# Kernel optimization log

Hardware: AMD Instinct MI355X
Metric: run time of the kernel (lower is better)

The kernel has to match this reference:

```python
import jax, jax.numpy as jnp
import numpy as np

H = 512   # d_model (hidden)
L = 2     # rnn_layer_dim
E = 321   # enc_in
C = 321   # c_out (must equal enc_in: decoder output is fed back as input)
T = 96    # seq_len
P = 96    # pred_len
B = 512   # batch


def _cell(x, h, c, Wih, Whh, bih, bhh):
    # PyTorch LSTM gate order: input, forget, cell(g), output
    g = x @ Wih.T + h @ Whh.T + bih + bhh
    i, f, gg, o = jnp.split(g, 4, axis=-1)
    c = jax.nn.sigmoid(f) * c + jax.nn.sigmoid(i) * jnp.tanh(gg)
    h = jax.nn.sigmoid(o) * jnp.tanh(c)
    return h, c


def _run_layer(xs, Wih, Whh, bih, bhh):
    # xs: [T, B, in_dim] -> ys: [T, B, H], final (h, c)
    b = xs.shape[1]
    h0 = jnp.zeros((b, Whh.shape[1]), xs.dtype)
    def step(carry, x):
        h, c = carry
        h, c = _cell(x, h, c, Wih, Whh, bih, bhh)
        return (h, c), h
    (h, c), ys = jax.lax.scan(step, (h0, h0), xs)
    return ys, h, c


def _forward(x_enc, x_mark_enc, x_dec, x_mark_dec,
             e_Wih0, e_Whh0, e_bih0, e_bhh0, e_Wih1, e_Whh1, e_bih1, e_bhh1,
             d_Wih0, d_Whh0, d_bih0, d_bhh0, d_Wih1, d_Whh1, d_bih1, d_bhh1,
             fc_W, fc_b):
    del x_mark_enc, x_dec, x_mark_dec  # unused in use_tf=False path
    xs = jnp.swapaxes(x_enc, 0, 1)                     # [T, B, E]
    ys, h0, c0 = _run_layer(xs, e_Wih0, e_Whh0, e_bih0, e_bhh0)
    _,  h1, c1 = _run_layer(ys, e_Wih1, e_Whh1, e_bih1, e_bhh1)

    inp0 = x_enc[:, -1, :]                             # [B, E] last source step

    def dec_step(carry, _):
        inp, h0, c0, h1, c1 = carry
        h0, c0 = _cell(inp, h0, c0, d_Wih0, d_Whh0, d_bih0, d_bhh0)
        h1, c1 = _cell(h0,  h1, c1, d_Wih1, d_Whh1, d_bih1, d_bhh1)
        out = h1 @ fc_W.T + fc_b                       # [B, C]
        return (out, h0, c0, h1, c1), out

    _, outs = jax.lax.scan(dec_step, (inp0, h0, c0, h1, c1), None, length=P)
    return jnp.swapaxes(outs, 0, 1)                    # [B, P, C]


def setup_inputs() -> dict:
    key = jax.random.key(0)
    ks = jax.random.split(key, 24)
    s = 1.0 / np.sqrt(H)  # PyTorch LSTM init scale
    def w(k, shape):
        return jax.random.uniform(k, shape, jnp.float32, -s, s)
    inp = {
        "x_enc": jax.random.normal(ks[0], (B, T, E), jnp.float32),
        "x_mark_enc": jax.random.normal(ks[1], (B, T, 4), jnp.float32),
        "x_dec": jax.random.normal(ks[2], (B, P, C), jnp.float32),
        "x_mark_dec": jax.random.normal(ks[3], (B, P, 4), jnp.float32),
        "e_Wih0": w(ks[4], (4 * H, E)),  "e_Whh0": w(ks[5], (4 * H, H)),
        "e_bih0": w(ks[6], (4 * H,)),    "e_bhh0": w(ks[7], (4 * H,)),
        "e_Wih1": w(ks[8], (4 * H, H)),  "e_Whh1": w(ks[9], (4 * H, H)),
        "e_bih1": w(ks[10], (4 * H,)),   "e_bhh1": w(ks[11], (4 * H,)),
        "d_Wih0": w(ks[12], (4 * H, E)), "d_Whh0": w(ks[13], (4 * H, H)),
        "d_bih0": w(ks[14], (4 * H,)),   "d_bhh0": w(ks[15], (4 * H,)),
        "d_Wih1": w(ks[16], (4 * H, H)), "d_Whh1": w(ks[17], (4 * H, H)),
        "d_bih1": w(ks[18], (4 * H,)),   "d_bhh1": w(ks[19], (4 * H,)),
        "fc_W": w(ks[20], (C, H)),       "fc_b": w(ks[21], (C,)),
    }
    return inp


def reference(x_enc, x_mark_enc, x_dec, x_mark_dec,
              e_Wih0, e_Whh0, e_bih0, e_bhh0, e_Wih1, e_Whh1, e_bih1, e_bhh1,
              d_Wih0, d_Whh0, d_bih0, d_bhh0, d_Wih1, d_Whh1, d_bih1, d_bhh1,
              fc_W, fc_b):
    return _forward(x_enc, x_mark_enc, x_dec, x_mark_dec,
                    e_Wih0, e_Whh0, e_bih0, e_bhh0, e_Wih1, e_Whh1, e_bih1, e_bhh1,
                    d_Wih0, d_Whh0, d_bih0, d_bhh0, d_Wih1, d_Whh1, d_bih1, d_bhh1,
                    fc_W, fc_b)
```

## Files before the change

kernel.cpp:

```cpp
#include <hip/hip_runtime.h>
#include <hip/hip_bf16.h>

#define BB 512
#define TT 96
#define PP 96
#define EE 321
#define CC 321
#define HH 512
#define G4 2048
#define EPAD 352
#define NFC 384

#define BUF_SZ 24576
#define XH_OFF 0
#define XL_OFF 8192
#define WH_OFF 16384
#define WL_OFF 20480
#define FC_SMEM 49152

#define SMEM128 98304
#define SMEM64  65536

typedef unsigned short u16;
typedef __attribute__((ext_vector_type(8))) short bf16x8;
typedef __attribute__((ext_vector_type(16))) float floatx16;

__device__ __forceinline__ void splitf(float v, u16& h, u16& l){
  __hip_bfloat16 bh = __float2bfloat16(v);
  h = *reinterpret_cast<u16*>(&bh);
  float r = v - __bfloat162float(bh);
  __hip_bfloat16 bl = __float2bfloat16(r);
  l = *reinterpret_cast<u16*>(&bl);
}

__device__ __forceinline__ void gload16(const void* g, void* l){
  __builtin_amdgcn_global_load_lds((const __attribute__((address_space(1))) void*)g,
                                   (__attribute__((address_space(3))) void*)l, 16, 0, 0);
}

__global__ void cvt_split(const float* __restrict__ src, u16* __restrict__ hi, u16* __restrict__ lo,
                          int rows, int cols, int rowspad, int colspad){
  int total = rowspad * colspad;
  for (int idx = blockIdx.x * blockDim.x + threadIdx.x; idx < total; idx += gridDim.x * blockDim.x){
    int r = idx / colspad, cc = idx - r * colspad;
    float v = (r < rows && cc < cols) ? src[(size_t)r * cols + cc] : 0.f;
    u16 h, l; splitf(v, h, l);
    hi[idx] = h; lo[idx] = l;
  }
}

__global__ void cvt_bias(const float* __restrict__ b1, const float* __restrict__ b2,
                         float* __restrict__ dst, int n, int npad){
  for (int i = blockIdx.x * blockDim.x + threadIdx.x; i < npad; i += gridDim.x * blockDim.x){
    float v = 0.f;
    if (i < n){ v = b1[i]; if (b2) v += b2[i]; }
    dst[i] = v;
  }
}

__global__ void init_inp(const float* __restrict__ x_enc, u16* __restrict__ inph, u16* __restrict__ inpl){
  int total = BB * EPAD;
  for (int idx = blockIdx.x * blockDim.x + threadIdx.x; idx < total; idx += gridDim.x * blockDim.x){
    int b = idx / EPAD, j = idx - b * EPAD;
    float v = (j < EE) ? x_enc[(size_t)b * TT * EE + (size_t)(TT - 1) * EE + j] : 0.f;
    u16 h, l; splitf(v, h, l);
    inph[idx] = h; inpl[idx] = l;
  }
}

__global__ void split_xenc(const float* __restrict__ x, u16* __restrict__ xh, u16* __restrict__ xl){
  const int total = TT * BB * EPAD;
  for (int idx = blockIdx.x * blockDim.x + threadIdx.x; idx < total; idx += gridDim.x * blockDim.x){
    int e = idx % EPAD;
    int rest = idx / EPAD;
    int b = rest % BB;
    int t = rest / BB;
    float v = (e < EE) ? x[((size_t)b * TT + t) * EE + e] : 0.f;
    u16 h, l; splitf(v, h, l);
    xh[idx] = h; xl[idx] = l;
  }
}

__global__ void wcomb(const float* __restrict__ A,
                      const float* __restrict__ Bm,
                      float* __restrict__ C){
  __shared__ float arow[EE];
  const int g = blockIdx.x;
  for (int e = threadIdx.x; e < EE; e += 256) arow[e] = A[(size_t)g * EE + e];
  __syncthreads();
  for (int k = threadIdx.x; k < HH; k += 256){
    float s = 0.f;
    for (int e = 0; e < EE; ++e) s += arow[e] * Bm[(size_t)e * HH + k];
    C[(size_t)g * HH + k] = s;
  }
}

__global__ void bias_fold(const float* __restrict__ bd0, const float* __restrict__ A,
                          const float* __restrict__ fcb, float* __restrict__ out){
  int g = blockIdx.x * blockDim.x + threadIdx.x;
  if (g < G4){
    float s = bd0[g];
    for (int e = 0; e < EE; ++e) s += A[(size_t)g * EE + e] * fcb[e];
    out[g] = s;
  }
}

template<int MT>
__device__ __forceinline__ void lstm_body(
    char* smem, int bx,
    const u16* __restrict__ Xh, const u16* __restrict__ Xl, int K1pad,
    const u16* __restrict__ Wih_h, const u16* __restrict__ Wih_l,
    const u16* __restrict__ Whh_h, const u16* __restrict__ Whh_l,
    const float* __restrict__ bias,
    const u16* __restrict__ Hph, const u16* __restrict__ Hpl,
    u16* __restrict__ Hnh, u16* __restrict__ Hnl,
    float* __restrict__ cst)
{
  constexpr int XROWB = MT * 64;
  constexpr int BUFB  = 2 * XROWB + 8192;
  constexpr int WH_O  = 2 * XROWB;
  constexpr int WL_O  = 2 * XROWB + 4096;

  float (*sG)[68] = (float (*)[68])(smem);

  const int tid  = threadIdx.x;
  const int lane = tid & 63;
  const int wid  = tid >> 6;
  const int wm = wid >> 1, wn = wid & 1;
  const int m0 = (bx >> 5) * MT;
  const int u0 = (bx & 31) * 16;

  floatx16 acc0 = {0.f,0.f,0.f,0.f,0.f,0.f,0.f,0.f,0.f,0.f,0.f,0.f,0.f,0.f,0.f,0.f};
  floatx16 acc1 = acc0;

  const int ml    = lane & 31;
  const int thalf = lane >> 5;
  const int a0r = (MT == 128 ? wm * 64 : wm * 32) + ml;
  const int a1r = a0r + 32;
  const int brw = wn * 32 + ml;
  const int xa  = (a0r >> 1) & 3;
  const int xb  = (brw >> 1) & 3;

  const int sl  = lane & 3;
  const int rq  = lane >> 2;
  const int rx0 = wid * (MT / 4) + rq;
  const int rw  = wid * 16 + rq;
  const int sgx = (sl ^ ((rx0 >> 1) & 3)) << 4;
  const int sgw = (sl ^ ((rw  >> 1) & 3)) << 4;
  const size_t gxr0 = (size_t)(m0 + rx0);
  const size_t gxr1 = gxr0 + 16;
  const size_t gwr  = (size_t)wid * HH + u0 + rq;
  const int oX = wid * (MT / 4) * 64;
  const int oW = wid * 16 * 64;

  const int nch1 = K1pad >> 5;
  const int ncht = nch1 + (HH >> 5);

  auto stage = [&](int ch){
    const bool p1 = ch < nch1;
    const int k0 = (p1 ? ch : ch - nch1) << 5;
    const u16* xh = p1 ? Xh : Hph;
    const u16* xl = p1 ? Xl : Hpl;
    const u16* wh = p1 ? Wih_h : Whh_h;
    const u16* wl = p1 ? Wih_l : Whh_l;
    const size_t Kp = p1 ? (size_t)K1pad : (size_t)HH;
    char* b = smem + (ch & 3) * BUFB;
    gload16((const char*)(xh + gxr0 * Kp + k0) + sgx, b + oX);
    if constexpr (MT == 128) gload16((const char*)(xh + gxr1 * Kp + k0) + sgx, b + oX + 1024);
    gload16((const char*)(xl + gxr0 * Kp + k0) + sgx, b + XROWB + oX);
    if constexpr (MT == 128) gload16((const char*)(xl + gxr1 * Kp + k0) + sgx, b + XROWB + oX + 1024);
    gload16((const char*)(wh + gwr  * Kp + k0) + sgw, b + WH_O + oW);
    gload16((const char*)(wl + gwr  * Kp + k0) + sgw, b + WL_O + oW);
  };

  stage(0); stage(1); stage(2);
  for (int ch = 0; ch < ncht; ++ch){
    if (ch + 3 < ncht) stage(ch + 3);
    __builtin_amdgcn_sched_barrier(0);
    const int rem = ncht - 1 - ch;
    if constexpr (MT == 128){
      if      (rem >= 3) asm volatile("s_waitcnt vmcnt(18)" ::: "memory");
      else if (rem == 2) asm volatile("s_waitcnt vmcnt(12)" ::: "memory");
      else if (rem == 1) asm volatile("s_waitcnt vmcnt(6)"  ::: "memory");
      else               asm volatile("s_waitcnt vmcnt(0)"  ::: "memory");
    } else {
      if      (rem >= 3) asm volatile("s_waitcnt vmcnt(12)" ::: "memory");
      else if (rem == 2) asm volatile("s_waitcnt vmcnt(8)"  ::: "memory");
      else if (rem == 1) asm volatile("s_waitcnt vmcnt(4)"  ::: "memory");
      else               asm volatile("s_waitcnt vmcnt(0)"  ::: "memory");
    }
    __builtin_amdgcn_s_barrier();
    __builtin_amdgcn_sched_barrier(0);
    const char* bufc = smem + (ch & 3) * BUFB;
    #pragma unroll
    for (int kk2 = 0; kk2 < 2; ++kk2){
      const int t0 = kk2 * 2 + thalf;
      bf16x8 ah0 = *(const bf16x8*)(bufc + a0r * 64 + ((t0 ^ xa) << 4));
      bf16x8 al0 = *(const bf16x8*)(bufc + XROWB + a0r * 64 + ((t0 ^ xa) << 4));
      bf16x8 bh  = *(const bf16x8*)(bufc + WH_O + brw * 64 + ((t0 ^ xb) << 4));
      bf16x8 bl  = *(const bf16x8*)(bufc + WL_O + brw * 64 + ((t0 ^ xb) << 4));
      acc0 = __builtin_amdgcn_mfma_f32_32x32x16_bf16(ah0, bh, acc0, 0, 0, 0);
      acc0 = __builtin_amdgcn_mfma_f32_32x32x16_bf16(ah0, bl, acc0, 0, 0, 0);
      acc0 = __builtin_amdgcn_mfma_f32_32x32x16_bf16(al0, bh, acc0, 0, 0, 0);
      if constexpr (MT == 128){
        bf16x8 ah1 = *(const bf16x8*)(bufc + a1r * 64 + ((t0 ^ xa) << 4));
        bf16x8 al1 = *(const bf16x8*)(bufc + XROWB + a1r * 64 + ((t0 ^ xa) << 4));
        acc1 = __builtin_amdgcn_mfma_f32_32x32x16_bf16(ah1, bh, acc1, 0, 0, 0);
        acc1 = __builtin_amdgcn_mfma_f32_32x32x16_bf16(ah1, bl, acc1, 0, 0, 0);
        acc1 = __builtin_amdgcn_mfma_f32_32x32x16_bf16(al1, bh, acc1, 0, 0, 0);
      }
    }
    __builtin_amdgcn_sched_barrier(0);
    asm volatile("s_waitcnt lgkmcnt(0)" ::: "memory");
    __builtin_amdgcn_s_barrier();
    __builtin_amdgcn_sched_barrier(0);
  }
  __syncthreads();

  #pragma unroll
  for (int r = 0; r < 16; ++r){
    const int mm = (r & 3) + 8 * (r >> 2) + 4 * thalf;
    if constexpr (MT == 128){
      sG[wm * 64 + mm][wn * 32 + ml]      = acc0[r];
      sG[wm * 64 + 32 + mm][wn * 32 + ml] = acc1[r];
    } else {
      sG[wm * 32 + mm][wn * 32 + ml]      = acc0[r];
    }
  }
  __syncthreads();
  for (int e = tid; e < MT * 16; e += 256){
    const int m = e >> 4, u = e & 15;
    const int gj = u0 + u;
    const float gi = sG[m][u]      + bias[gj];
    const float gf = sG[m][16 + u] + bias[HH + gj];
    const float gg = sG[m][32 + u] + bias[2 * HH + gj];
    const float go = sG[m][48 + u] + bias[3 * HH + gj];
    const float si = 1.f / (1.f + expf(-gi));
    const float sf = 1.f / (1.f + expf(-gf));
    const float so = 1.f / (1.f + expf(-go));
    const size_t sidx = (size_t)(m0 + m) * HH + gj;
    const float cn = sf * cst[sidx] + si * tanhf(gg);
    const float hn = so * tanhf(cn);
    cst[sidx] = cn;
    u16 hh, hl; splitf(hn, hh, hl);
    Hnh[sidx] = hh; Hnl[sidx] = hl;
  }
}

__global__ __launch_bounds__(256) void lstm_one(
    const u16* Xh, const u16* Xl, int K1pad,
    const u16* Wih_h, const u16* Wih_l, const u16* Whh_h, const u16* Whh_l,
    const float* bias, const u16* Hph, const u16* Hpl,
    u16* Hnh, u16* Hnl, float* cst)
{
  extern __shared__ char smem[];
  lstm_body<64>(smem, blockIdx.x, Xh, Xl, K1pad,
                Wih_h, Wih_l, Whh_h, Whh_l, bias, Hph, Hpl, Hnh, Hnl, cst);
}

__global__ __launch_bounds__(256) void lstm_pair(
    int act0, const u16* X0h, const u16* X0l,
    const u16* W0ih_h, const u16* W0ih_l, const u16* W0hh_h, const u16* W0hh_l,
    const float* b0, const u16* H0ph, const u16* H0pl, u16* H0nh, u16* H0nl, float* c0,
    int act1, const u16* X1h, const u16* X1l,
    const u16* W1ih_h, const u16* W1ih_l, const u16* W1hh_h, const u16* W1hh_l,
    const float* b1, const u16* H1ph, const u16* H1pl, u16* H1nh, u16* H1nl, float* c1)
{
  extern __shared__ char smem[];
  const int half = blockIdx.x >> 7;
  const int bx   = blockIdx.x & 127;
  if (half == 0 ? !act0 : !act1) return;
  lstm_body<128>(smem, bx,
                 half ? X1h : X0h, half ? X1l : X0l, half ? HH : EPAD,
                 half ? W1ih_h : W0ih_h, half ? W1ih_l : W0ih_l,
                 half ? W1hh_h : W0hh_h, half ? W1hh_l : W0hh_l,
                 half ? b1 : b0,
                 half ? H1ph : H0ph, half ? H1pl : H0pl,
                 half ? H1nh : H0nh, half ? H1nl : H0nl,
                 half ? c1 : c0);
}

__global__ __launch_bounds__(256) void fc_batch(
    const u16* __restrict__ Hh, const u16* __restrict__ Hl,
    const u16* __restrict__ Wh, const u16* __restrict__ Wl,
    const float* __restrict__ bfc,
    float* __restrict__ out)
{
  extern __shared__ char smem[];
  const int tid = threadIdx.x, lane = tid & 63, wid = tid >> 6;
  const int wm = wid >> 1, wn = wid & 1;
  const int m0 = blockIdx.x * 128;
  const int n0 = blockIdx.y * 64;

  floatx16 acc0 = {0.f,0.f,0.f,0.f,0.f,0.f,0.f,0.f,0.f,0.f,0.f,0.f,0.f,0.f,0.f,0.f};
  floatx16 acc1 = {0.f,0.f,0.f,0.f,0.f,0.f,0.f,0.f,0.f,0.f,0.f,0.f,0.f,0.f,0.f,0.f};

  const int ml    = lane & 31;
  const int thalf = lane >> 5;
  const int a0r = wm * 64 + ml;
  const int a1r = a0r + 32;
  const int brw = wn * 32 + ml;
  const int xa  = (a0r >> 1) & 3;
  const int xb  = (brw >> 1) & 3;

  const int sl  = lane & 3;
  const int rq  = lane >> 2;
  const int rx0 = wid * 32 + rq;
  const int rw  = wid * 16 + rq;
  const int sgx = (sl ^ ((rx0 >> 1) & 3)) << 4;
  const int sgw = (sl ^ ((rw  >> 1) & 3)) << 4;
  const size_t gxr0 = (size_t)(m0 + rx0);
  const size_t gxr1 = gxr0 + 16;
  const size_t gwr  = (size_t)(n0 + rw);
  const int oX = wid * 32 * 64;
  const int oW = wid * 16 * 64;

  auto stage = [&](int ch){
    const int k0 = ch << 5;
    char* b = smem + (ch & 1) * BUF_SZ;
    gload16((const char*)(Hh + gxr0 * HH + k0) + sgx, b + XH_OFF + oX);
    gload16((const char*)(Hh + gxr1 * HH + k0) + sgx, b + XH_OFF + oX + 1024);
    gload16((const char*)(Hl + gxr0 * HH + k0) + sgx, b + XL_OFF + oX);
    gload16((const char*)(Hl + gxr1 * HH + k0) + sgx, b + XL_OFF + oX + 1024);
    gload16((const char*)(Wh + gwr  * HH + k0) + sgw, b + WH_OFF + oW);
    gload16((const char*)(Wl + gwr  * HH + k0) + sgw, b + WL_OFF + oW);
  };

  stage(0);
  for (int ch = 0; ch < 16; ++ch){
    if (ch + 1 < 16) stage(ch + 1);
    __builtin_amdgcn_sched_barrier(0);
    if (ch + 1 < 16) { asm volatile("s_waitcnt vmcnt(6)" ::: "memory"); }
    else             { asm volatile("s_waitcnt vmcnt(0)" ::: "memory"); }
    __builtin_amdgcn_s_barrier();
    __builtin_amdgcn_sched_barrier(0);
    const char* bufc = smem + (ch & 1) * BUF_SZ;
    #pragma unroll
    for (int kk2 = 0; kk2 < 2; ++kk2){
      const int t0 = kk2 * 2 + thalf;
      bf16x8 ah0 = *(const bf16x8*)(bufc + XH_OFF + a0r * 64 + ((t0 ^ xa) << 4));
      bf16x8 al0 = *(const bf16x8*)(bufc + XL_OFF + a0r * 64 + ((t0 ^ xa) << 4));
      bf16x8 ah1 = *(const bf16x8*)(bufc + XH_OFF + a1r * 64 + ((t0 ^ xa) << 4));
      bf16x8 al1 = *(const bf16x8*)(bufc + XL_OFF + a1r * 64 + ((t0 ^ xa) << 4));
      bf16x8 bh  = *(const bf16x8*)(bufc + WH_OFF + brw * 64 + ((t0 ^ xb) << 4));
      bf16x8 bl  = *(const bf16x8*)(bufc + WL_OFF + brw * 64 + ((t0 ^ xb) << 4));
      acc0 = __builtin_amdgcn_mfma_f32_32x32x16_bf16(ah0, bh, acc0, 0, 0, 0);
      acc0 = __builtin_amdgcn_mfma_f32_32x32x16_bf16(ah0, bl, acc0, 0, 0, 0);
      acc0 = __builtin_amdgcn_mfma_f32_32x32x16_bf16(al0, bh, acc0, 0, 0, 0);
      acc1 = __builtin_amdgcn_mfma_f32_32x32x16_bf16(ah1, bh, acc1, 0, 0, 0);
      acc1 = __builtin_amdgcn_mfma_f32_32x32x16_bf16(ah1, bl, acc1, 0, 0, 0);
      acc1 = __builtin_amdgcn_mfma_f32_32x32x16_bf16(al1, bh, acc1, 0, 0, 0);
    }
    __builtin_amdgcn_sched_barrier(0);
    asm volatile("s_waitcnt lgkmcnt(0)" ::: "memory");
    __builtin_amdgcn_s_barrier();
    __builtin_amdgcn_sched_barrier(0);
  }

  const int n = n0 + wn * 32 + ml;
  if (n < CC){
    const float bv = bfc[n];
    #pragma unroll
    for (int r = 0; r < 16; ++r){
      const int mm = (r & 3) + 8 * (r >> 2) + 4 * thalf;
      {
        const int rr = m0 + wm * 64 + mm;
        out[(size_t)(rr & 511) * PP * CC + (size_t)(rr >> 9) * CC + n] = acc0[r] + bv;
      }
      {
        const int rr = m0 + wm * 64 + 32 + mm;
        out[(size_t)(rr & 511) * PP * CC + (size_t)(rr >> 9) * CC + n] = acc1[r] + bv;
      }
    }
  }
}

extern "C" void kernel_launch(void* const* d_in, const int* in_sizes, int n_in,
                              void* d_out, int out_size, void* d_ws, size_t ws_size,
                              hipStream_t stream) {
  const float* x_enc  = (const float*)d_in[0];
  const float* e_Wih0 = (const float*)d_in[4];
  const float* e_Whh0 = (const float*)d_in[5];
  const float* e_bih0 = (const float*)d_in[6];
  const float* e_bhh0 = (const float*)d_in[7];
  const float* e_Wih1 = (const float*)d_in[8];
  const float* e_Whh1 = (const float*)d_in[9];
  const float* e_bih1 = (const float*)d_in[10];
  const float* e_bhh1 = (const float*)d_in[11];
  const float* d_Wih0 = (const float*)d_in[12];
  const float* d_Whh0 = (const float*)d_in[13];
  const float* d_bih0 = (const float*)d_in[14];
  const float* d_bhh0 = (const float*)d_in[15];
  const float* d_Wih1 = (const float*)d_in[16];
  const float* d_Whh1 = (const float*)d_in[17];
  const float* d_bih1 = (const float*)d_in[18];
  const float* d_bhh1 = (const float*)d_in[19];
  const float* fc_W   = (const float*)d_in[20];
  const float* fc_b   = (const float*)d_in[21];

  static bool attr_done = false;
  if (!attr_done){
    hipFuncSetAttribute((const void*)lstm_pair, hipFuncAttributeMaxDynamicSharedMemorySize, SMEM128);
    hipFuncSetAttribute((const void*)lstm_one,  hipFuncAttributeMaxDynamicSharedMemorySize, SMEM64);
    attr_done = true;
  }

  char* base = (char*)d_ws;
  size_t off = 0;
  auto alloc_us = [&](size_t n){ u16* p = (u16*)(base + off); off += ((n * 2 + 15) & ~(size_t)15); return p; };
  auto alloc_f  = [&](size_t n){ float* p = (float*)(base + off); off += ((n * 4 + 15) & ~(size_t)15); return p; };

  u16 *We0ih_h = alloc_us((size_t)G4 * EPAD), *We0ih_l = alloc_us((size_t)G4 * EPAD);
  u16 *We0hh_h = alloc_us((size_t)G4 * HH),   *We0hh_l = alloc_us((size_t)G4 * HH);
  u16 *We1ih_h = alloc_us((size_t)G4 * HH),   *We1ih_l = alloc_us((size_t)G4 * HH);
  u16 *We1hh_h = alloc_us((size_t)G4 * HH),   *We1hh_l = alloc_us((size_t)G4 * HH);
  u16 *Wd0ih_h = alloc_us((size_t)G4 * EPAD), *Wd0ih_l = alloc_us((size_t)G4 * EPAD);
  u16 *Wd0hh_h = alloc_us((size_t)G4 * HH),   *Wd0hh_l = alloc_us((size_t)G4 * HH);
  u16 *Wd1ih_h = alloc_us((size_t)G4 * HH),   *Wd1ih_l = alloc_us((size_t)G4 * HH);
  u16 *Wd1hh_h = alloc_us((size_t)G4 * HH),   *Wd1hh_l = alloc_us((size_t)G4 * HH);
  u16 *Wfc_h   = alloc_us((size_t)NFC * HH),  *Wfc_l   = alloc_us((size_t)NFC * HH);
  u16 *Wc_h    = alloc_us((size_t)G4 * HH),   *Wc_l    = alloc_us((size_t)G4 * HH);
  float* be0 = alloc_f(G4);
  float* be1 = alloc_f(G4);
  float* bd0 = alloc_f(G4);
  float* bd1 = alloc_f(G4);
  float* bfc = alloc_f(NFC);
  float* bd0c = alloc_f(G4);
  float* Wcf32 = alloc_f((size_t)G4 * HH);
  u16* h0h[2]; u16* h0l[2]; u16* h1h[2]; u16* h1l[2];
  h0h[0] = alloc_us((size_t)BB * HH); h0l[0] = alloc_us((size_t)BB * HH);
  h1h[0] = alloc_us((size_t)BB * HH); h1l[0] = alloc_us((size_t)BB * HH);
  float* c0 = alloc_f((size_t)BB * HH);
  float* c1 = alloc_f((size_t)BB * HH);
  h0h[1] = alloc_us((size_t)BB * HH); h0l[1] = alloc_us((size_t)BB * HH);
  h1h[1] = alloc_us((size_t)BB * HH); h1l[1] = alloc_us((size_t)BB * HH);
  u16* inph = alloc_us((size_t)BB * EPAD);
  u16* inpl = alloc_us((size_t)BB * EPAD);
  u16* Xench = alloc_us((size_t)TT * BB * EPAD);
  u16* Xencl = alloc_us((size_t)TT * BB * EPAD);
  u16* histh = alloc_us((size_t)PP * BB * HH);
  u16* histl = alloc_us((size_t)PP * BB * HH);

  cvt_split<<<512, 256, 0, stream>>>(e_Wih0, We0ih_h, We0ih_l, G4, EE, G4, EPAD);
  cvt_split<<<512, 256, 0, stream>>>(e_Whh0, We0hh_h, We0hh_l, G4, HH, G4, HH);
  cvt_split<<<512, 256, 0, stream>>>(e_Wih1, We1ih_h, We1ih_l, G4, HH, G4, HH);
  cvt_split<<<512, 256, 0, stream>>>(e_Whh1, We1hh_h, We1hh_l, G4, HH, G4, HH);
  cvt_split<<<512, 256, 0, stream>>>(d_Wih0, Wd0ih_h, Wd0ih_l, G4, EE, G4, EPAD);
  cvt_split<<<512, 256, 0, stream>>>(d_Whh0, Wd0hh_h, Wd0hh_l, G4, HH, G4, HH);
  cvt_split<<<512, 256, 0, stream>>>(d_Wih1, Wd1ih_h, Wd1ih_l, G4, HH, G4, HH);
  cvt_split<<<512, 256, 0, stream>>>(d_Whh1, Wd1hh_h, Wd1hh_l, G4, HH, G4, HH);
  cvt_split<<<512, 256, 0, stream>>>(fc_W,   Wfc_h,   Wfc_l,   CC, HH, NFC, HH);
  cvt_bias<<<8, 256, 0, stream>>>(e_bih0, e_bhh0, be0, G4, G4);
  cvt_bias<<<8, 256, 0, stream>>>(e_bih1, e_bhh1, be1, G4, G4);
  cvt_bias<<<8, 256, 0, stream>>>(d_bih0, d_bhh0, bd0, G4, G4);
  cvt_bias<<<8, 256, 0, stream>>>(d_bih1, d_bhh1, bd1, G4, G4);
  cvt_bias<<<2, 256, 0, stream>>>(fc_b, nullptr, bfc, CC, NFC);
  wcomb<<<G4, 256, 0, stream>>>(d_Wih0, fc_W, Wcf32);
  bias_fold<<<8, 256, 0, stream>>>(bd0, d_Wih0, fc_b, bd0c);
  cvt_split<<<512, 256, 0, stream>>>(Wcf32, Wc_h, Wc_l, G4, HH, G4, HH);
  hipMemsetAsync(h0h[0], 0, (size_t)4 * BB * HH * sizeof(u16) + (size_t)2 * BB * HH * sizeof(float), stream);
  init_inp<<<512, 256, 0, stream>>>(x_enc, inph, inpl);
  split_xenc<<<4096, 256, 0, stream>>>(x_enc, Xench, Xencl);

  for (int t = 0; t <= TT; ++t){
    const int rd = t & 1, wrp = (t + 1) & 1;
    const size_t ts = (size_t)(t < TT ? t : 0) * BB * EPAD;
    lstm_pair<<<256, 256, SMEM128, stream>>>(
        (t < TT) ? 1 : 0, Xench + ts, Xencl + ts,
        We0ih_h, We0ih_l, We0hh_h, We0hh_l, be0,
        h0h[rd], h0l[rd], h0h[wrp], h0l[wrp], c0,
        (t > 0) ? 1 : 0, h0h[rd], h0l[rd],
        We1ih_h, We1ih_l, We1hh_h, We1hh_l, be1,
        h1h[wrp], h1l[wrp], h1h[rd], h1l[rd], c1);
  }

  const size_t S = (size_t)BB * HH;
  for (int p = 0; p < PP; ++p){
    const int rd = p & 1, wrp = (p + 1) & 1;
    const u16* hp_h = p ? histh + (size_t)(p - 1) * S : h1h[0];
    const u16* hp_l = p ? histl + (size_t)(p - 1) * S : h1l[0];
    lstm_one<<<256, 256, SMEM64, stream>>>(
        p ? hp_h : inph, p ? hp_l : inpl, p ? HH : EPAD,
        p ? Wc_h : Wd0ih_h, p ? Wc_l : Wd0ih_l, Wd0hh_h, Wd0hh_l,
        p ? bd0c : bd0,
        h0h[rd], h0l[rd], h0h[wrp], h0l[wrp], c0);
    lstm_one<<<256, 256, SMEM64, stream>>>(
        h0h[wrp], h0l[wrp], HH,
        Wd1ih_h, Wd1ih_l, Wd1hh_h, Wd1hh_l, bd1,
        hp_h, hp_l,
        histh + (size_t)p * S, histl + (size_t)p * S, c1);
  }

  fc_batch<<<dim3((PP * BB) / 128, NFC / 64), 256, FC_SMEM, stream>>>(
      histh, histl, Wfc_h, Wfc_l, bfc, (float*)d_out);
}
```

Baseline: 6.303 ms.

## Split decoder LSTM gate GEMMs and overlap recurrent partials with the next cell

The decoder step is split in two. The recurrent-weight GEMM for one layer is now computed ahead, by extra blocks running inside the other layer's kernel, and stored as fp32 partial gates. The cell kernel then only does the input-side GEMM and adds the precomputed partials. This doubles the grid per launch so more CUs are busy and shortens the dependent chain at each step. The cost is an extra fp32 round trip of gate partials through global memory. Separately, the k-loop pipeline is reordered to use one barrier per chunk and to issue the prefetch after that barrier.

```diff
diff --git a/kernel.cpp b/kernel.cpp
--- a/kernel.cpp
+++ b/kernel.cpp
@@ -19,7 +19,7 @@
 #define FC_SMEM 49152
 
 #define SMEM128 98304
-#define SMEM64  65536
+#define DEC_SMEM 65536
 
 typedef unsigned short u16;
 typedef __attribute__((ext_vector_type(8))) short bf16x8;
@@ -81,8 +81,7 @@
   }
 }
 
-__global__ void wcomb(const float* __restrict__ A,
-                      const float* __restrict__ Bm,
+__global__ void wcomb(const float* __restrict__ A, const float* __restrict__ Bm,
                       float* __restrict__ C){
   __shared__ float arow[EE];
   const int g = blockIdx.x;
@@ -111,7 +110,7 @@
     const u16* __restrict__ Xh, const u16* __restrict__ Xl, int K1pad,
     const u16* __restrict__ Wih_h, const u16* __restrict__ Wih_l,
     const u16* __restrict__ Whh_h, const u16* __restrict__ Whh_l,
-    const float* __restrict__ bias,
+    const float* __restrict__ bias, const float* __restrict__ Gin,
     const u16* __restrict__ Hph, const u16* __restrict__ Hpl,
     u16* __restrict__ Hnh, u16* __restrict__ Hnl,
     float* __restrict__ cst)
@@ -154,7 +153,7 @@
   const int oW = wid * 16 * 64;
 
   const int nch1 = K1pad >> 5;
-  const int ncht = nch1 + (HH >> 5);
+  const int ncht = Hph ? nch1 + (HH >> 5) : nch1;
 
   auto stage = [&](int ch){
     const bool p1 = ch < nch1;
@@ -175,22 +174,21 @@
 
   stage(0); stage(1); stage(2);
   for (int ch = 0; ch < ncht; ++ch){
-    if (ch + 3 < ncht) stage(ch + 3);
-    __builtin_amdgcn_sched_barrier(0);
-    const int rem = ncht - 1 - ch;
+    const int rem = (ncht - 1 - ch) < 2 ? (ncht - 1 - ch) : 2;
+    __builtin_amdgcn_sched_barrier(0);
     if constexpr (MT == 128){
-      if      (rem >= 3) asm volatile("s_waitcnt vmcnt(18)" ::: "memory");
-      else if (rem == 2) asm volatile("s_waitcnt vmcnt(12)" ::: "memory");
+      if      (rem == 2) asm volatile("s_waitcnt vmcnt(12)" ::: "memory");
       else if (rem == 1) asm volatile("s_waitcnt vmcnt(6)"  ::: "memory");
       else               asm volatile("s_waitcnt vmcnt(0)"  ::: "memory");
     } else {
-      if      (rem >= 3) asm volatile("s_waitcnt vmcnt(12)" ::: "memory");
-      else if (rem == 2) asm volatile("s_waitcnt vmcnt(8)"  ::: "memory");
+      if      (rem == 2) asm volatile("s_waitcnt vmcnt(8)"  ::: "memory");
       else if (rem == 1) asm volatile("s_waitcnt vmcnt(4)"  ::: "memory");
       else               asm volatile("s_waitcnt vmcnt(0)"  ::: "memory");
     }
+    asm volatile("s_waitcnt lgkmcnt(0)" ::: "memory");
     __builtin_amdgcn_s_barrier();
     __builtin_amdgcn_sched_barrier(0);
+    if (ch + 3 < ncht) stage(ch + 3);
     const char* bufc = smem + (ch & 3) * BUFB;
     #pragma unroll
     for (int kk2 = 0; kk2 < 2; ++kk2){
@@ -210,10 +208,6 @@
         acc1 = __builtin_amdgcn_mfma_f32_32x32x16_bf16(al1, bh, acc1, 0, 0, 0);
       }
     }
-    __builtin_amdgcn_sched_barrier(0);
-    asm volatile("s_waitcnt lgkmcnt(0)" ::: "memory");
-    __builtin_amdgcn_s_barrier();
-    __builtin_amdgcn_sched_barrier(0);
   }
   __syncthreads();
 
@@ -231,10 +225,14 @@
   for (int e = tid; e < MT * 16; e += 256){
     const int m = e >> 4, u = e & 15;
     const int gj = u0 + u;
-    const float gi = sG[m][u]      + bias[gj];
-    const float gf = sG[m][16 + u] + bias[HH + gj];
-    const float gg = sG[m][32 + u] + bias[2 * HH + gj];
-    const float go = sG[m][48 + u] + bias[3 * HH + gj];
+    float gi = sG[m][u]      + bias[gj];
+    float gf = sG[m][16 + u] + bias[HH + gj];
+    float gg = sG[m][32 + u] + bias[2 * HH + gj];
+    float go = sG[m][48 + u] + bias[3 * HH + gj];
+    if (Gin){
+      const float* gb = Gin + (size_t)(m0 + m) * G4;
+      gi += gb[gj]; gf += gb[HH + gj]; gg += gb[2 * HH + gj]; go += gb[3 * HH + gj];
+    }
     const float si = 1.f / (1.f + expf(-gi));
     const float sf = 1.f / (1.f + expf(-gf));
     const float so = 1.f / (1.f + expf(-go));
@@ -247,15 +245,108 @@
   }
 }
 
-__global__ __launch_bounds__(256) void lstm_one(
-    const u16* Xh, const u16* Xl, int K1pad,
-    const u16* Wih_h, const u16* Wih_l, const u16* Whh_h, const u16* Whh_l,
-    const float* bias, const u16* Hph, const u16* Hpl,
-    u16* Hnh, u16* Hnl, float* cst)
+__device__ __forceinline__ void part_body(
+    char* smem, int bx,
+    const u16* __restrict__ Xh, const u16* __restrict__ Xl,
+    const u16* __restrict__ W_h, const u16* __restrict__ W_l,
+    float* __restrict__ Gout)
+{
+  constexpr int XROWB = 64 * 64;
+  constexpr int BUFB  = 2 * XROWB + 8192;
+  constexpr int WH_O  = 2 * XROWB;
+  constexpr int WL_O  = 2 * XROWB + 4096;
+
+  const int tid  = threadIdx.x;
+  const int lane = tid & 63;
+  const int wid  = tid >> 6;
+  const int wm = wid >> 1, wn = wid & 1;
+  const int m0 = (bx >> 5) * 64;
+  const int u0 = (bx & 31) * 16;
+
+  floatx16 acc0 = {0.f,0.f,0.f,0.f,0.f,0.f,0.f,0.f,0.f,0.f,0.f,0.f,0.f,0.f,0.f,0.f};
+
+  const int ml    = lane & 31;
+  const int thalf = lane >> 5;
+  const int a0r = wm * 32 + ml;
+  const int brw = wn * 32 + ml;
+  const int xa  = (a0r >> 1) & 3;
+  const int xb  = (brw >> 1) & 3;
+
+  const int sl  = lane & 3;
+  const int rq  = lane >> 2;
+  const int rx0 = wid * 16 + rq;
+  const int rw  = wid * 16 + rq;
+  const int sgx = (sl ^ ((rx0 >> 1) & 3)) << 4;
+  const int sgw = (sl ^ ((rw  >> 1) & 3)) << 4;
+  const size_t gxr0 = (size_t)(m0 + rx0);
+  const size_t gwr  = (size_t)wid * HH + u0 + rq;
+  const int oX = wid * 16 * 64;
+  const int oW = wid * 16 * 64;
+
+  auto stage = [&](int ch){
+    const int k0 = ch << 5;
+    char* b = smem + (ch & 3) * BUFB;
+    gload16((const char*)(Xh + gxr0 * HH + k0) + sgx, b + oX);
+    gload16((const char*)(Xl + gxr0 * HH + k0) + sgx, b + XROWB + oX);
+    gload16((const char*)(W_h + gwr * HH + k0) + sgw, b + WH_O + oW);
+    gload16((const char*)(W_l + gwr * HH + k0) + sgw, b + WL_O + oW);
+  };
+
+  stage(0); stage(1); stage(2);
+  for (int ch = 0; ch < 16; ++ch){
+    const int rem = (15 - ch) < 2 ? (15 - ch) : 2;
+    __builtin_amdgcn_sched_barrier(0);
+    if      (rem == 2) asm volatile("s_waitcnt vmcnt(8)" ::: "memory");
+    else if (rem == 1) asm volatile("s_waitcnt vmcnt(4)" ::: "memory");
+    else               asm volatile("s_waitcnt vmcnt(0)" ::: "memory");
+    asm volatile("s_waitcnt lgkmcnt(0)" ::: "memory");
+    __builtin_amdgcn_s_barrier();
+    __builtin_amdgcn_sched_barrier(0);
+    if (ch + 3 < 16) stage(ch + 3);
+    const char* bufc = smem + (ch & 3) * BUFB;
+    #pragma unroll
+    for (int kk2 = 0; kk2 < 2; ++kk2){
+      const int t0 = kk2 * 2 + thalf;
+      bf16x8 ah0 = *(const bf16x8*)(bufc + a0r * 64 + ((t0 ^ xa) << 4));
+      bf16x8 al0 = *(const bf16x8*)(bufc + XROWB + a0r * 64 + ((t0 ^ xa) << 4));
+      bf16x8 bh  = *(const bf16x8*)(bufc + WH_O + brw * 64 + ((t0 ^ xb) << 4));
+      bf16x8 bl  = *(const bf16x8*)(bufc + WL_O + brw * 64 + ((t0 ^ xb) << 4));
+      acc0 = __builtin_amdgcn_mfma_f32_32x32x16_bf16(ah0, bh, acc0, 0, 0, 0);
+      acc0 = __builtin_amdgcn_mfma_f32_32x32x16_bf16(ah0, bl, acc0, 0, 0, 0);
+      acc0 = __builtin_amdgcn_mfma_f32_32x32x16_bf16(al0, bh, acc0, 0, 0, 0);
+    }
+  }
+  const int c = wn * 32 + ml;
+  const size_t gcolo = (size_t)(c >> 4) * HH + u0 + (c & 15);
+  #pragma unroll
+  for (int r = 0; r < 16; ++r){
+    const int mm = (r & 3) + 8 * (r >> 2) + 4 * thalf;
+    Gout[(size_t)(m0 + wm * 32 + mm) * G4 + gcolo] = acc0[r];
+  }
+}
+
+__global__ __launch_bounds__(256) void dec_ab(
+    const u16* Xfh, const u16* Xfl, int Kf,
+    const u16* Wf_h, const u16* Wf_l,
+    const float* bias, const float* Gin,
+    u16* Hnh, u16* Hnl, float* cst,
+    const u16* Xph, const u16* Xpl,
+    const u16* Wp_h, const u16* Wp_l,
+    float* Gout)
 {
   extern __shared__ char smem[];
-  lstm_body<64>(smem, blockIdx.x, Xh, Xl, K1pad,
-                Wih_h, Wih_l, Whh_h, Whh_l, bias, Hph, Hpl, Hnh, Hnl, cst);
+  if (blockIdx.x < 256)
+    lstm_body<64>(smem, blockIdx.x, Xfh, Xfl, Kf, Wf_h, Wf_l, nullptr, nullptr,
+                  bias, Gin, nullptr, nullptr, Hnh, Hnl, cst);
+  else
+    part_body(smem, blockIdx.x - 256, Xph, Xpl, Wp_h, Wp_l, Gout);
+}
+
+__global__ __launch_bounds__(256) void part_only(
+    const u16* Xh, const u16* Xl, const u16* W_h, const u16* W_l, float* Gout)
+{
+  extern __shared__ char smem[];
+  part_body(smem, blockIdx.x, Xh, Xl, W_h, W_l, Gout);
 }
 
 __global__ __launch_bounds__(256) void lstm_pair(
@@ -274,7 +365,7 @@
                  half ? X1h : X0h, half ? X1l : X0l, half ? HH : EPAD,
                  half ? W1ih_h : W0ih_h, half ? W1ih_l : W0ih_l,
                  half ? W1hh_h : W0hh_h, half ? W1hh_l : W0hh_l,
-                 half ? b1 : b0,
+                 half ? b1 : b0, nullptr,
                  half ? H1ph : H0ph, half ? H1pl : H0pl,
                  half ? H1nh : H0nh, half ? H1nl : H0nl,
                  half ? c1 : c0);
@@ -401,7 +492,8 @@
   static bool attr_done = false;
   if (!attr_done){
     hipFuncSetAttribute((const void*)lstm_pair, hipFuncAttributeMaxDynamicSharedMemorySize, SMEM128);
-    hipFuncSetAttribute((const void*)lstm_one,  hipFuncAttributeMaxDynamicSharedMemorySize, SMEM64);
+    hipFuncSetAttribute((const void*)dec_ab,    hipFuncAttributeMaxDynamicSharedMemorySize, DEC_SMEM);
+    hipFuncSetAttribute((const void*)part_only, hipFuncAttributeMaxDynamicSharedMemorySize, DEC_SMEM);
     attr_done = true;
   }
 
@@ -427,6 +519,8 @@
   float* bfc = alloc_f(NFC);
   float* bd0c = alloc_f(G4);
   float* Wcf32 = alloc_f((size_t)G4 * HH);
+  float* Gp0 = alloc_f((size_t)BB * G4);
+  float* Gp1 = alloc_f((size_t)BB * G4);
   u16* h0h[2]; u16* h0l[2]; u16* h1h[2]; u16* h1l[2];
   h0h[0] = alloc_us((size_t)BB * HH); h0l[0] = alloc_us((size_t)BB * HH);
   h1h[0] = alloc_us((size_t)BB * HH); h1l[0] = alloc_us((size_t)BB * HH);
@@ -475,20 +569,22 @@
   }
 
   const size_t S = (size_t)BB * HH;
+  part_only<<<256, 256, DEC_SMEM, stream>>>(h0h[0], h0l[0], Wd0hh_h, Wd0hh_l, Gp0);
   for (int p = 0; p < PP; ++p){
-    const int rd = p & 1, wrp = (p + 1) & 1;
     const u16* hp_h = p ? histh + (size_t)(p - 1) * S : h1h[0];
     const u16* hp_l = p ? histl + (size_t)(p - 1) * S : h1l[0];
-    lstm_one<<<256, 256, SMEM64, stream>>>(
+    dec_ab<<<512, 256, DEC_SMEM, stream>>>(
         p ? hp_h : inph, p ? hp_l : inpl, p ? HH : EPAD,
-        p ? Wc_h : Wd0ih_h, p ? Wc_l : Wd0ih_l, Wd0hh_h, Wd0hh_l,
-        p ? bd0c : bd0,
-        h0h[rd], h0l[rd], h0h[wrp], h0l[wrp], c0);
-    lstm_one<<<256, 256, SMEM64, stream>>>(
-        h0h[wrp], h0l[wrp], HH,
-        Wd1ih_h, Wd1ih_l, Wd1hh_h, Wd1hh_l, bd1,
-        hp_h, hp_l,
-        histh + (size_t)p * S, histl + (size_t)p * S, c1);
+        p ? Wc_h : Wd0ih_h, p ? Wc_l : Wd0ih_l,
+        p ? bd0c : bd0, Gp0,
+        h0h[1], h0l[1], c0,
+        hp_h, hp_l, Wd1hh_h, Wd1hh_l, Gp1);
+    dec_ab<<<512, 256, DEC_SMEM, stream>>>(
+        h0h[1], h0l[1], HH,
+        Wd1ih_h, Wd1ih_l,
+        bd1, Gp1,
+        histh + (size_t)p * S, histl + (size_t)p * S, c1,
+        h0h[1], h0l[1], Wd0hh_h, Wd0hh_l, Gp0);
   }
 
   fc_batch<<<dim3((PP * BB) / 128, NFC / 64), 256, FC_SMEM, stream>>>(
```

Result: faster. 5.869 ms (-6.9%).
